# Kernel tuning notes

Measured on AMD Instinct MI355X. Metric: run time of the kernel, lower is better.

The kernel has to match this reference:

```python
import jax, jax.numpy as jnp
import numpy as np

B, IN, H, NC = 8192, 1024, 1024, 16
CS = H // NC  # chunk_size = 64


def cumsoftmax(x):
    # cumulative softmax along last dim
    return jnp.cumsum(jax.nn.softmax(x, axis=-1), axis=-1)


def setup_inputs() -> dict:
    key = jax.random.key(0)
    ks = jax.random.split(key, 9)
    s_ih = 1.0 / np.sqrt(IN)
    s_hh = 1.0 / np.sqrt(H)
    return {
        "x": jax.random.normal(ks[0], (B, IN), jnp.float32),
        "hx": jax.random.normal(ks[1], (B, H), jnp.float32),
        "cx": jax.random.normal(ks[2], (B, NC, CS), jnp.float32),
        "input_floor": jax.random.normal(ks[3], (B, NC), jnp.float32),
        "forget_floor": jax.random.normal(ks[4], (B, NC), jnp.float32),
        "W_ih": jax.random.uniform(ks[5], (4 * H, IN), jnp.float32, -s_ih, s_ih),
        "b_ih": jax.random.uniform(ks[6], (4 * H,), jnp.float32, -s_ih, s_ih),
        "W_hh": jax.random.uniform(ks[7], (4 * H, H), jnp.float32, -s_hh, s_hh),
        "b_hh": jax.random.uniform(ks[8], (4 * H,), jnp.float32, -s_hh, s_hh),
    }


def reference(x, hx, cx, input_floor, forget_floor, W_ih, b_ih, W_hh, b_hh):
    # dual GEMM (eval path: dropconnect=0.0 -> plain linear)
    gates = x @ W_ih.T + b_ih + hx @ W_hh.T + b_hh          # [B, 4H]
    g = gates.reshape(-1, NC * 4, CS)                        # [B, 4*NC, CS]
    outgate, cell, ingate, forgetgate = jnp.split(g, 4, axis=1)  # each [B, NC, CS]

    happy_in, sad_in = jnp.split(input_floor, 2, axis=1)     # [B, NC/2] each
    happy_fg, sad_fg = jnp.split(forget_floor, 2, axis=1)

    happy_cingate = cumsoftmax(happy_in)
    happy_cforgetgate = jnp.flip(cumsoftmax(jnp.flip(happy_fg, 1)), 1)
    sad_cingate = jnp.flip(cumsoftmax(jnp.flip(sad_in, 1)), 1)
    sad_cforgetgate = cumsoftmax(sad_fg)

    cingate = jnp.concatenate([happy_cingate, sad_cingate], axis=1)[:, :, None]      # [B, NC, 1]
    cforgetgate = jnp.concatenate([happy_cforgetgate, sad_cforgetgate], axis=1)[:, :, None]

    ingate = jax.nn.sigmoid(ingate)
    forgetgate = jax.nn.sigmoid(forgetgate)
    cell = jnp.tanh(cell)
    outgate = jax.nn.sigmoid(outgate)

    overlap = cforgetgate * cingate
    forgetgate = forgetgate * overlap + (cforgetgate - overlap)
    ingate = ingate * overlap + (cingate - overlap)

    cy = forgetgate * cx + ingate * cell                     # [B, NC, CS]
    hy = outgate * jnp.tanh(cy)
    return hy.reshape(-1, H), cy
```

## Files before the change

kernel.cpp:

```cpp
#include <hip/hip_runtime.h>
#include <hip/hip_bf16.h>


#define B_ROWS 8192
#define IN_DIM 1024
#define H_DIM  1024
#define NCHUNK 16
#define K_TOT  2048

#define BM   256
#define BN   256
#define BK   64
#define NKT  (K_TOT / BK)
#define THREADS 512

#define A_PACK_BYTES ((size_t)B_ROWS * K_TOT * 2)
#define W_PACK_BYTES ((size_t)16 * 256 * K_TOT * 2)

typedef __attribute__((ext_vector_type(4))) float  f32x4;
typedef __bf16 bf16x8 __attribute__((ext_vector_type(8)));

__device__ __forceinline__ float sigmoidf_(float x) {
    return 1.0f / (1.0f + __expf(-x));
}
__device__ __forceinline__ float tanhf_(float x) {
    float e = __expf(-2.0f * fabsf(x));
    float t = (1.0f - e) / (1.0f + e);
    return copysignf(t, x);
}

__device__ __forceinline__ void gload16(const __bf16* gsrc, __bf16* lds_dst) {
    __builtin_amdgcn_global_load_lds(
        (const __attribute__((address_space(1))) unsigned int*)gsrc,
        (__attribute__((address_space(3))) unsigned int*)lds_dst, 16, 0, 0);
}

__device__ __forceinline__ bf16x8 cvt8(f32x4 v0, f32x4 v1) {
    bf16x8 o;
    o[0] = (__bf16)v0.x; o[1] = (__bf16)v0.y; o[2] = (__bf16)v0.z; o[3] = (__bf16)v0.w;
    o[4] = (__bf16)v1.x; o[5] = (__bf16)v1.y; o[6] = (__bf16)v1.z; o[7] = (__bf16)v1.w;
    return o;
}

__global__ __launch_bounds__(256)
void pack_A(const float* __restrict__ x, const float* __restrict__ hx,
            __bf16* __restrict__ Abf)
{
    int idx = blockIdx.x * 256 + threadIdx.x;
    int row = idx >> 8;
    int c8  = (idx & 255) << 3;
    const float* src = (c8 < IN_DIM)
        ? (x  + (size_t)row * IN_DIM + c8)
        : (hx + (size_t)row * IN_DIM + (c8 - IN_DIM));
    f32x4 v0 = *reinterpret_cast<const f32x4*>(src);
    f32x4 v1 = *reinterpret_cast<const f32x4*>(src + 4);
    *reinterpret_cast<bf16x8*>(Abf + (size_t)row * K_TOT + c8) = cvt8(v0, v1);
}

__global__ __launch_bounds__(256)
void pack_W(const float* __restrict__ W_ih, const float* __restrict__ W_hh,
            __bf16* __restrict__ Wp)
{
    int idx = blockIdx.x * 256 + threadIdx.x;
    int k8  = (idx & 255) << 3;
    int n   = (idx >> 8) & 255;
    int bh  = idx >> 16;
    int g   = (n >> 4) & 3;
    int j   = (n >> 6) * 16 + (n & 15);
    int wr  = g * H_DIM + bh * 64 + j;
    const float* src = (k8 < IN_DIM)
        ? (W_ih + (size_t)wr * IN_DIM + k8)
        : (W_hh + (size_t)wr * IN_DIM + (k8 - IN_DIM));
    f32x4 v0 = *reinterpret_cast<const f32x4*>(src);
    f32x4 v1 = *reinterpret_cast<const f32x4*>(src + 4);
    *reinterpret_cast<bf16x8*>(Wp + ((size_t)bh * 256 + n) * K_TOT + k8) = cvt8(v0, v1);
}

__device__ __forceinline__ void stage_half(const __bf16* __restrict__ gbase, int kb,
                                           __bf16* lbase, int row0, int tid) {
    #pragma unroll
    for (int i = 0; i < 2; ++i) {
        int e   = i * 4096 + tid * 8;
        int row = row0 + (e >> 6);
        int kd  = e & 63;
        gload16(gbase + (size_t)row * K_TOT + kb + (kd ^ ((row & 7) << 3)), lbase + e);
    }
}

#define PH(q) \
    __builtin_amdgcn_s_setprio(1); \
    _Pragma("unroll") \
    for (int fn = 0; fn < 4; ++fn) { \
        acc[2*(q)][fn]   = __builtin_amdgcn_mfma_f32_16x16x32_bf16(af[2*(q)][0],   bfr[fn][0], acc[2*(q)][fn],   0,0,0); \
        acc[2*(q)][fn]   = __builtin_amdgcn_mfma_f32_16x16x32_bf16(af[2*(q)][1],   bfr[fn][1], acc[2*(q)][fn],   0,0,0); \
        acc[2*(q)+1][fn] = __builtin_amdgcn_mfma_f32_16x16x32_bf16(af[2*(q)+1][0], bfr[fn][0], acc[2*(q)+1][fn], 0,0,0); \
        acc[2*(q)+1][fn] = __builtin_amdgcn_mfma_f32_16x16x32_bf16(af[2*(q)+1][1], bfr[fn][1], acc[2*(q)+1][fn], 0,0,0); \
    } \
    __builtin_amdgcn_s_setprio(0);

#define PHASE(q, ...) { \
    __VA_ARGS__; \
    asm volatile("" ::: "memory"); \
    __builtin_amdgcn_s_barrier(); \
    asm volatile("s_waitcnt lgkmcnt(0)" ::: "memory"); \
    __builtin_amdgcn_sched_barrier(0); \
    PH(q) \
    asm volatile("" ::: "memory"); \
    __builtin_amdgcn_s_barrier(); \
    asm volatile("" ::: "memory"); \
}

#define PHASE_V(q, ...) { \
    __VA_ARGS__; \
    asm volatile("" ::: "memory"); \
    __builtin_amdgcn_s_barrier(); \
    asm volatile("s_waitcnt lgkmcnt(0)" ::: "memory"); \
    __builtin_amdgcn_sched_barrier(0); \
    PH(q) \
    asm volatile("s_waitcnt vmcnt(6)" ::: "memory"); \
    __builtin_amdgcn_s_barrier(); \
    asm volatile("" ::: "memory"); \
}

#define LOAD_FRAGS(As, Bs) { \
    _Pragma("unroll") \
    for (int fn = 0; fn < 4; ++fn) { \
        int br = wcol + fn * 16 + lr; \
        bfr[fn][0] = *reinterpret_cast<const bf16x8*>(&(Bs)[br * 64 + ((lh*8)      ^ ((br & 7) << 3))]); \
        bfr[fn][1] = *reinterpret_cast<const bf16x8*>(&(Bs)[br * 64 + ((32 + lh*8) ^ ((br & 7) << 3))]); \
    } \
    _Pragma("unroll") \
    for (int mm = 0; mm < 8; ++mm) { \
        int ar = wrow + mm * 16 + lr; \
        af[mm][0] = *reinterpret_cast<const bf16x8*>(&(As)[ar * 64 + ((lh*8)      ^ ((ar & 7) << 3))]); \
        af[mm][1] = *reinterpret_cast<const bf16x8*>(&(As)[ar * 64 + ((32 + lh*8) ^ ((ar & 7) << 3))]); \
    } }

__global__ __launch_bounds__(THREADS, 2)
void onlstm_gemm8(const __bf16* __restrict__ Abf, const __bf16* __restrict__ Wp,
                  const float* __restrict__ cx,
                  const float* __restrict__ input_floor,
                  const float* __restrict__ forget_floor,
                  const float* __restrict__ b_ih, const float* __restrict__ b_hh,
                  float* __restrict__ out)
{
    __shared__ __align__(16) __bf16 lds[65536];
    __shared__ float ci_s[BM], cf_s[BM], bias_s[BN];

    const int tid = threadIdx.x;
    const int n0  = blockIdx.x;
    const int swz = (n0 & 7) * 64 + (n0 >> 3);
    const int bh  = swz >> 5;
    const int bm  = swz & 31;
    const int h0  = bh * 64;
    const int nc  = bh;

    if (tid < BM) {
        {
            int g = (tid >> 4) & 3;
            int j = (tid >> 6) * 16 + (tid & 15);
            int wr = g * H_DIM + h0 + j;
            bias_s[tid] = b_ih[wr] + b_hh[wr];
        }
        int b = bm * BM + tid;
        const int off = (nc < 8) ? 0 : 8;
        const int ic  = (nc < 8) ? nc : (nc - 8);
        const float* pin = input_floor  + (size_t)b * NCHUNK + off;
        const float* pfg = forget_floor + (size_t)b * NCHUNK + off;
        float vi[8], vf[8];
        float mi = -1e30f, mf = -1e30f;
        #pragma unroll
        for (int t = 0; t < 8; ++t) {
            vi[t] = pin[t]; vf[t] = pfg[t];
            mi = fmaxf(mi, vi[t]); mf = fmaxf(mf, vf[t]);
        }
        float si = 0.f, sf = 0.f;
        #pragma unroll
        for (int t = 0; t < 8; ++t) {
            vi[t] = __expf(vi[t] - mi); vf[t] = __expf(vf[t] - mf);
            si += vi[t]; sf += vf[t];
        }
        float pi = 0.f, pf = 0.f;
        #pragma unroll
        for (int t = 0; t < 8; ++t) { if (t <= ic) { pi += vi[t]; pf += vf[t]; } }
        float suf_i = si - pi + vi[ic];
        float suf_f = sf - pf + vf[ic];
        float civ, cfv;
        if (nc < 8) { civ = pi / si;    cfv = suf_f / sf; }
        else        { civ = suf_i / si; cfv = pf / sf;    }
        ci_s[tid] = civ; cf_s[tid] = cfv;
    }

    const __bf16* Arow = Abf + (size_t)(bm * BM) * K_TOT;
    const __bf16* Wblk = Wp  + (size_t)bh * 256 * K_TOT;
    __bf16* const A0p = lds;
    __bf16* const B0p = lds + 16384;
    __bf16* const A1p = lds + 32768;
    __bf16* const B1p = lds + 49152;

    stage_half(Arow, 0,  A0p,        0,   tid);
    stage_half(Arow, 0,  A0p + 8192, 128, tid);
    stage_half(Wblk, 0,  B0p,        0,   tid);
    stage_half(Wblk, 0,  B0p + 8192, 128, tid);
    stage_half(Arow, BK, A1p,        0,   tid);
    stage_half(Arow, BK, A1p + 8192, 128, tid);
    stage_half(Wblk, BK, B1p,        0,   tid);
    asm volatile("s_waitcnt lgkmcnt(0)" ::: "memory");
    asm volatile("s_waitcnt vmcnt(6)"   ::: "memory");
    __builtin_amdgcn_s_barrier();
    asm volatile("" ::: "memory");

    f32x4  acc[8][4];
    #pragma unroll
    for (int i = 0; i < 8; ++i)
        #pragma unroll
        for (int j = 0; j < 4; ++j) acc[i][j] = (f32x4){0.f, 0.f, 0.f, 0.f};
    bf16x8 af[8][2];
    bf16x8 bfr[4][2];

    const int l    = tid & 63;
    const int wid  = tid >> 6;
    const int wr   = wid >> 2;
    const int wc   = wid & 3;
    const int lr   = l & 15;
    const int lh   = l >> 4;
    const int wrow = wr * 128;
    const int wcol = wc * 64;

    #pragma unroll 1
    for (int it = 0; it < NKT / 2; ++it) {
        const int t = 2 * it;
        LOAD_FRAGS(A0p, B0p);
        PHASE  (0, stage_half(Wblk, ((t+1) & 31) * BK, B1p + 8192, 128, tid));
        PHASE  (1, stage_half(Arow, ((t+2) & 31) * BK, A0p,        0,   tid));
        PHASE  (2, stage_half(Arow, ((t+2) & 31) * BK, A0p + 8192, 128, tid));
        PHASE_V(3, stage_half(Wblk, ((t+2) & 31) * BK, B0p,        0,   tid));
        LOAD_FRAGS(A1p, B1p);
        PHASE  (0, stage_half(Wblk, ((t+2) & 31) * BK, B0p + 8192, 128, tid));
        PHASE  (1, stage_half(Arow, ((t+3) & 31) * BK, A1p,        0,   tid));
        PHASE  (2, stage_half(Arow, ((t+3) & 31) * BK, A1p + 8192, 128, tid));
        PHASE_V(3, stage_half(Wblk, ((t+3) & 31) * BK, B1p,        0,   tid));
    }
    asm volatile("s_waitcnt vmcnt(0)" ::: "memory");

    const size_t CY_OFF = (size_t)B_ROWS * H_DIM;
    const int hcol = h0 + wc * 16 + lr;
    #pragma unroll
    for (int m = 0; m < 8; ++m) {
        #pragma unroll
        for (int r = 0; r < 4; ++r) {
            int rt = wrow + m * 16 + lh * 4 + r;
            int b  = bm * BM + rt;
            float civ = ci_s[rt], cfv = cf_s[rt];
            float ovl = cfv * civ;
            float og = acc[m][0][r] + bias_s[wcol + lr];
            float cg = acc[m][1][r] + bias_s[wcol + 16 + lr];
            float ig = acc[m][2][r] + bias_s[wcol + 32 + lr];
            float fg = acc[m][3][r] + bias_s[wcol + 48 + lr];
            float i_s = sigmoidf_(ig);
            float f_s = sigmoidf_(fg);
            float c_t = tanhf_(cg);
            float o_s = sigmoidf_(og);
            float fq = f_s * ovl + (cfv - ovl);
            float iq = i_s * ovl + (civ - ovl);
            float cxv = cx[(size_t)b * H_DIM + hcol];
            float cyv = fq * cxv + iq * c_t;
            float hyv = o_s * tanhf_(cyv);
            out[(size_t)b * H_DIM + hcol] = hyv;
            out[CY_OFF + (size_t)b * H_DIM + hcol] = cyv;
        }
    }
}

extern "C" void kernel_launch(void* const* d_in, const int* in_sizes, int n_in,
                              void* d_out, int out_size, void* d_ws, size_t ws_size,
                              hipStream_t stream) {
    const float* x            = (const float*)d_in[0];
    const float* hx           = (const float*)d_in[1];
    const float* cx           = (const float*)d_in[2];
    const float* input_floor  = (const float*)d_in[3];
    const float* forget_floor = (const float*)d_in[4];
    const float* W_ih         = (const float*)d_in[5];
    const float* b_ih         = (const float*)d_in[6];
    const float* W_hh         = (const float*)d_in[7];
    const float* b_hh         = (const float*)d_in[8];
    float* out = (float*)d_out;

    __bf16* Abf = (__bf16*)d_ws;
    __bf16* Wp  = (__bf16*)((char*)d_ws + A_PACK_BYTES);
    pack_A<<<B_ROWS, 256, 0, stream>>>(x, hx, Abf);
    pack_W<<<16 * 256, 256, 0, stream>>>(W_ih, W_hh, Wp);
    onlstm_gemm8<<<512, THREADS, 0, stream>>>(
        Abf, Wp, cx, input_floor, forget_floor, b_ih, b_hh, out);
}
```

Before: 178.1 us.

## Interleave per-phase A fragment loads with MFMA and restage prefetch order

Restructures the main GEMM loop so that A fragments are read from LDS per phase (two 16-row tiles at a time) instead of all eight up front. This shrinks the A fragment register array from 8x2 to 2x2, which lowers register pressure and spreads LDS reads across the MFMA phases. The prefetch schedule is also reordered: the prologue now stages the two W halves for the next tile instead of A, each phase prefetches the next A tile or the W tile after it, and the vmcnt threshold changes accordingly. The block-index mapping changes so that consecutive blocks cover 8x4 groups of row tiles within the same weight column block, aimed at better L2 reuse of the weights. The main risk is less ILP, because each phase now waits on its own LDS reads before issuing MFMAs.

```diff
diff --git a/kernel.cpp b/kernel.cpp
--- a/kernel.cpp
+++ b/kernel.cpp
@@ -87,54 +87,50 @@
     }
 }
 
-#define PH(q) \
+#define SWZ(r, k) ((r) * 64 + ((k) ^ (((r) & 7) << 3)))
+
+#define LDB(Bs) { \
+    _Pragma("unroll") \
+    for (int fn = 0; fn < 4; ++fn) { \
+        int br = wcol + fn * 16 + lr; \
+        bfr[fn][0] = *reinterpret_cast<const bf16x8*>(&(Bs)[SWZ(br, lh * 8)]); \
+        bfr[fn][1] = *reinterpret_cast<const bf16x8*>(&(Bs)[SWZ(br, 32 + lh * 8)]); \
+    } }
+
+#define LDA(As, q) { \
+    int ar = wrow + (q) * 32 + lr; \
+    af[0][0] = *reinterpret_cast<const bf16x8*>(&(As)[SWZ(ar, lh * 8)]); \
+    af[0][1] = *reinterpret_cast<const bf16x8*>(&(As)[SWZ(ar, 32 + lh * 8)]); \
+    af[1][0] = *reinterpret_cast<const bf16x8*>(&(As)[SWZ(ar + 16, lh * 8)]); \
+    af[1][1] = *reinterpret_cast<const bf16x8*>(&(As)[SWZ(ar + 16, 32 + lh * 8)]); \
+    }
+
+#define PH_PRE \
+    asm volatile("" ::: "memory"); \
+    __builtin_amdgcn_s_barrier(); \
+    asm volatile("s_waitcnt lgkmcnt(0)" ::: "memory"); \
+    __builtin_amdgcn_sched_barrier(0);
+
+#define MF(q) { \
     __builtin_amdgcn_s_setprio(1); \
     _Pragma("unroll") \
     for (int fn = 0; fn < 4; ++fn) { \
-        acc[2*(q)][fn]   = __builtin_amdgcn_mfma_f32_16x16x32_bf16(af[2*(q)][0],   bfr[fn][0], acc[2*(q)][fn],   0,0,0); \
-        acc[2*(q)][fn]   = __builtin_amdgcn_mfma_f32_16x16x32_bf16(af[2*(q)][1],   bfr[fn][1], acc[2*(q)][fn],   0,0,0); \
-        acc[2*(q)+1][fn] = __builtin_amdgcn_mfma_f32_16x16x32_bf16(af[2*(q)+1][0], bfr[fn][0], acc[2*(q)+1][fn], 0,0,0); \
-        acc[2*(q)+1][fn] = __builtin_amdgcn_mfma_f32_16x16x32_bf16(af[2*(q)+1][1], bfr[fn][1], acc[2*(q)+1][fn], 0,0,0); \
+        acc[2*(q)][fn]   = __builtin_amdgcn_mfma_f32_16x16x32_bf16(af[0][0], bfr[fn][0], acc[2*(q)][fn],   0,0,0); \
+        acc[2*(q)][fn]   = __builtin_amdgcn_mfma_f32_16x16x32_bf16(af[0][1], bfr[fn][1], acc[2*(q)][fn],   0,0,0); \
+        acc[2*(q)+1][fn] = __builtin_amdgcn_mfma_f32_16x16x32_bf16(af[1][0], bfr[fn][0], acc[2*(q)+1][fn], 0,0,0); \
+        acc[2*(q)+1][fn] = __builtin_amdgcn_mfma_f32_16x16x32_bf16(af[1][1], bfr[fn][1], acc[2*(q)+1][fn], 0,0,0); \
     } \
-    __builtin_amdgcn_s_setprio(0);
-
-#define PHASE(q, ...) { \
-    __VA_ARGS__; \
+    __builtin_amdgcn_s_setprio(0); \
+    __builtin_amdgcn_sched_barrier(0); \
+}
+
+#define PH_POST \
     asm volatile("" ::: "memory"); \
-    __builtin_amdgcn_s_barrier(); \
-    asm volatile("s_waitcnt lgkmcnt(0)" ::: "memory"); \
-    __builtin_amdgcn_sched_barrier(0); \
-    PH(q) \
-    asm volatile("" ::: "memory"); \
-    __builtin_amdgcn_s_barrier(); \
-    asm volatile("" ::: "memory"); \
-}
-
-#define PHASE_V(q, ...) { \
-    __VA_ARGS__; \
-    asm volatile("" ::: "memory"); \
-    __builtin_amdgcn_s_barrier(); \
-    asm volatile("s_waitcnt lgkmcnt(0)" ::: "memory"); \
-    __builtin_amdgcn_sched_barrier(0); \
-    PH(q) \
-    asm volatile("s_waitcnt vmcnt(6)" ::: "memory"); \
-    __builtin_amdgcn_s_barrier(); \
-    asm volatile("" ::: "memory"); \
-}
-
-#define LOAD_FRAGS(As, Bs) { \
-    _Pragma("unroll") \
-    for (int fn = 0; fn < 4; ++fn) { \
-        int br = wcol + fn * 16 + lr; \
-        bfr[fn][0] = *reinterpret_cast<const bf16x8*>(&(Bs)[br * 64 + ((lh*8)      ^ ((br & 7) << 3))]); \
-        bfr[fn][1] = *reinterpret_cast<const bf16x8*>(&(Bs)[br * 64 + ((32 + lh*8) ^ ((br & 7) << 3))]); \
-    } \
-    _Pragma("unroll") \
-    for (int mm = 0; mm < 8; ++mm) { \
-        int ar = wrow + mm * 16 + lr; \
-        af[mm][0] = *reinterpret_cast<const bf16x8*>(&(As)[ar * 64 + ((lh*8)      ^ ((ar & 7) << 3))]); \
-        af[mm][1] = *reinterpret_cast<const bf16x8*>(&(As)[ar * 64 + ((32 + lh*8) ^ ((ar & 7) << 3))]); \
-    } }
+    __builtin_amdgcn_s_barrier();
+
+#define PH_POSTV \
+    asm volatile("s_waitcnt vmcnt(4)" ::: "memory"); \
+    __builtin_amdgcn_s_barrier();
 
 __global__ __launch_bounds__(THREADS, 2)
 void onlstm_gemm8(const __bf16* __restrict__ Abf, const __bf16* __restrict__ Wp,
@@ -149,9 +145,8 @@
 
     const int tid = threadIdx.x;
     const int n0  = blockIdx.x;
-    const int swz = (n0 & 7) * 64 + (n0 >> 3);
-    const int bh  = swz >> 5;
-    const int bm  = swz & 31;
+    const int bm  = (n0 & 7) * 4 + ((n0 >> 3) & 3);
+    const int bh  = n0 >> 5;
     const int h0  = bh * 64;
     const int nc  = bh;
 
@@ -159,8 +154,8 @@
         {
             int g = (tid >> 4) & 3;
             int j = (tid >> 6) * 16 + (tid & 15);
-            int wr = g * H_DIM + h0 + j;
-            bias_s[tid] = b_ih[wr] + b_hh[wr];
+            int wrr = g * H_DIM + h0 + j;
+            bias_s[tid] = b_ih[wrr] + b_hh[wrr];
         }
         int b = bm * BM + tid;
         const int off = (nc < 8) ? 0 : 8;
@@ -202,11 +197,10 @@
     stage_half(Arow, 0,  A0p + 8192, 128, tid);
     stage_half(Wblk, 0,  B0p,        0,   tid);
     stage_half(Wblk, 0,  B0p + 8192, 128, tid);
-    stage_half(Arow, BK, A1p,        0,   tid);
-    stage_half(Arow, BK, A1p + 8192, 128, tid);
     stage_half(Wblk, BK, B1p,        0,   tid);
+    stage_half(Wblk, BK, B1p + 8192, 128, tid);
     asm volatile("s_waitcnt lgkmcnt(0)" ::: "memory");
-    asm volatile("s_waitcnt vmcnt(6)"   ::: "memory");
+    asm volatile("s_waitcnt vmcnt(0)"   ::: "memory");
     __builtin_amdgcn_s_barrier();
     asm volatile("" ::: "memory");
 
@@ -215,31 +209,45 @@
     for (int i = 0; i < 8; ++i)
         #pragma unroll
         for (int j = 0; j < 4; ++j) acc[i][j] = (f32x4){0.f, 0.f, 0.f, 0.f};
-    bf16x8 af[8][2];
+    bf16x8 af[2][2];
     bf16x8 bfr[4][2];
 
     const int l    = tid & 63;
     const int wid  = tid >> 6;
-    const int wr   = wid >> 2;
+    const int wrw  = wid >> 2;
     const int wc   = wid & 3;
     const int lr   = l & 15;
     const int lh   = l >> 4;
-    const int wrow = wr * 128;
+    const int wrow = wrw * 128;
     const int wcol = wc * 64;
 
     #pragma unroll 1
     for (int it = 0; it < NKT / 2; ++it) {
         const int t = 2 * it;
-        LOAD_FRAGS(A0p, B0p);
-        PHASE  (0, stage_half(Wblk, ((t+1) & 31) * BK, B1p + 8192, 128, tid));
-        PHASE  (1, stage_half(Arow, ((t+2) & 31) * BK, A0p,        0,   tid));
-        PHASE  (2, stage_half(Arow, ((t+2) & 31) * BK, A0p + 8192, 128, tid));
-        PHASE_V(3, stage_half(Wblk, ((t+2) & 31) * BK, B0p,        0,   tid));
-        LOAD_FRAGS(A1p, B1p);
-        PHASE  (0, stage_half(Wblk, ((t+2) & 31) * BK, B0p + 8192, 128, tid));
-        PHASE  (1, stage_half(Arow, ((t+3) & 31) * BK, A1p,        0,   tid));
-        PHASE  (2, stage_half(Arow, ((t+3) & 31) * BK, A1p + 8192, 128, tid));
-        PHASE_V(3, stage_half(Wblk, ((t+3) & 31) * BK, B1p,        0,   tid));
+        LDB(B0p); LDA(A0p, 0);
+        stage_half(Arow, ((t + 1) & 31) * BK, A1p,        0,   tid);
+        PH_PRE; MF(0); PH_POST;
+        LDA(A0p, 1);
+        stage_half(Arow, ((t + 1) & 31) * BK, A1p + 8192, 128, tid);
+        PH_PRE; MF(1); PH_POST;
+        LDA(A0p, 2);
+        stage_half(Wblk, ((t + 2) & 31) * BK, B0p,        0,   tid);
+        PH_PRE; MF(2); PH_POST;
+        LDA(A0p, 3);
+        stage_half(Wblk, ((t + 2) & 31) * BK, B0p + 8192, 128, tid);
+        PH_PRE; MF(3); PH_POSTV;
+        LDB(B1p); LDA(A1p, 0);
+        stage_half(Arow, ((t + 2) & 31) * BK, A0p,        0,   tid);
+        PH_PRE; MF(0); PH_POST;
+        LDA(A1p, 1);
+        stage_half(Arow, ((t + 2) & 31) * BK, A0p + 8192, 128, tid);
+        PH_PRE; MF(1); PH_POST;
+        LDA(A1p, 2);
+        stage_half(Wblk, ((t + 3) & 31) * BK, B1p,        0,   tid);
+        PH_PRE; MF(2); PH_POST;
+        LDA(A1p, 3);
+        stage_half(Wblk, ((t + 3) & 31) * BK, B1p + 8192, 128, tid);
+        PH_PRE; MF(3); PH_POSTV;
     }
     asm volatile("s_waitcnt vmcnt(0)" ::: "memory");
 
```

After: 160.4 us. 1.11x faster.
